# Kernel optimization log

Hardware: AMD Instinct MI355X
Metric: run time of the kernel (lower is better)

The kernel has to match this reference:

```python
import jax, jax.numpy as jnp
import numpy as np
import math

B, T, D_MODEL, H = 2, 2048, 1024, 16
HD = D_MODEL // H  # head_dim = 64


def setup_inputs() -> dict:
    key = jax.random.key(0)
    ks = jax.random.split(key, 9)
    inp = {
        "x_q": jax.random.normal(ks[0], (B, T, D_MODEL), dtype=jnp.float32),
        "x_k": jax.random.normal(ks[1], (B, T, D_MODEL), dtype=jnp.float32),
        "x_v": jax.random.normal(ks[2], (B, T, D_MODEL), dtype=jnp.float32),
        "mask": jax.random.randint(ks[3], (B, T), 0, 2, dtype=jnp.int32),
        "causal": 1,
        "relative_position_bias": jax.random.normal(ks[4], (1, H, T, T), dtype=jnp.float32),
        "Wq": jax.random.normal(ks[5], (D_MODEL, D_MODEL), dtype=jnp.float32) * 0.02,
        "Wk": jax.random.normal(ks[6], (D_MODEL, D_MODEL), dtype=jnp.float32) * 0.02,
        "Wv": jax.random.normal(ks[7], (D_MODEL, D_MODEL), dtype=jnp.float32) * 0.02,
        "Wo": jax.random.normal(ks[8], (D_MODEL, D_MODEL), dtype=jnp.float32) * 0.02,
    }
    return inp


def _split_heads(x):
    b, t, _ = x.shape
    return x.reshape(b, t, H, HD).transpose(0, 2, 1, 3)  # (B, H, T, HD)


def reference(x_q, x_k, x_v, mask, causal, relative_position_bias, Wq, Wk, Wv, Wo):
    # torch.nn.Linear: y = x @ W.T
    q = _split_heads(x_q @ Wq.T)
    k = _split_heads(x_k @ Wk.T)
    v = _split_heads(x_v @ Wv.T)

    # padding mask (B, T_k) -> (B, 1, 1, T_k), combined with causal tril
    attn_mask = mask[:, None, None, :]
    if causal:
        tril = jnp.tril(jnp.ones((T, T), dtype=jnp.int32))[None, None]
        attn_mask = attn_mask & tril

    scores = jnp.einsum('bhqd,bhkd->bhqk', q, k) / math.sqrt(HD)
    scores = scores + relative_position_bias
    scores = jnp.where(attn_mask == 0, jnp.float32(-1e9), scores)
    attn = jax.nn.softmax(scores, axis=-1)  # (B, H, Tq, Tk)

    out_h = jnp.einsum('bhqk,bhkd->bhqd', attn, v)
    out = out_h.transpose(0, 2, 1, 3).reshape(B, T, D_MODEL)
    out = out @ Wo.T
    return out, attn
```

## Files before the change

kernel.cpp:

```cpp
#include <hip/hip_runtime.h>
#include <hip/hip_bf16.h>
#include <hip/hip_fp16.h>

#define B_ 2
#define T_ 2048
#define DM 1024
#define H_ 16
#define HD_ 64

typedef __attribute__((ext_vector_type(8))) short bf16x8v;
typedef __attribute__((ext_vector_type(4))) short short4v;
typedef __attribute__((ext_vector_type(4))) float f32x4;

__device__ __forceinline__ short f2bf(float f){
  unsigned u = __builtin_bit_cast(unsigned, f);
  u += 0x7fffu + ((u >> 16) & 1u);
  return (short)(u >> 16);
}
__device__ __forceinline__ float bf2f(short s){
  unsigned u = ((unsigned)(unsigned short)s) << 16;
  return __builtin_bit_cast(float, u);
}

#define GLOAD_LDS16(g, l) \
  __builtin_amdgcn_global_load_lds((const __attribute__((address_space(1))) unsigned int*)(g), \
                                   (__attribute__((address_space(3))) unsigned int*)(l), 16, 0, 0)

#define MFMA16(a, b, c) __builtin_amdgcn_mfma_f32_16x16x32_bf16((a), (b), (c), 0, 0, 0)

__global__ __launch_bounds__(256) void conv_kernel(
    const float* __restrict__ s0, const float* __restrict__ s1, const float* __restrict__ s2,
    const float* __restrict__ s3, const float* __restrict__ s4, const float* __restrict__ s5,
    const float* __restrict__ s6,
    short* __restrict__ d0, short* __restrict__ d1, short* __restrict__ d2,
    short* __restrict__ d3, short* __restrict__ d4, short* __restrict__ d5,
    short* __restrict__ d6)
{
  int y = blockIdx.y;
  const float* s; short* d; int n;
  switch (y) {
    case 0: s = s0; d = d0; n = B_*T_*DM; break;
    case 1: s = s1; d = d1; n = B_*T_*DM; break;
    case 2: s = s2; d = d2; n = B_*T_*DM; break;
    case 3: s = s3; d = d3; n = DM*DM;   break;
    case 4: s = s4; d = d4; n = DM*DM;   break;
    case 5: s = s5; d = d5; n = DM*DM;   break;
    default: s = s6; d = d6; n = DM*DM;  break;
  }
  int i = (blockIdx.x * 256 + threadIdx.x) * 4;
  if (i >= n) return;
  float4 f = *(const float4*)(s + i);
  short4v o;
  o.x = f2bf(f.x); o.y = f2bf(f.y); o.z = f2bf(f.z); o.w = f2bf(f.w);
  *(short4v*)(d + i) = o;
}

__global__ __launch_bounds__(256) void proj_gemm(
    const short* __restrict__ xq, const short* __restrict__ xk, const short* __restrict__ xv,
    const short* __restrict__ wq, const short* __restrict__ wk, const short* __restrict__ wv,
    short* __restrict__ qo, short* __restrict__ ko, short* __restrict__ vto)
{
  __shared__ short As[128 * 32];
  __shared__ short Bs[128 * 32];
  const int z = blockIdx.z;
  const short* A  = (z == 0) ? xq : (z == 1) ? xk : xv;
  const short* Bw = (z == 0) ? wq : (z == 1) ? wk : wv;
  const int m0 = blockIdx.x * 128;
  const int n0 = blockIdx.y * 128;
  const int tid = threadIdx.x;
  const int w = tid >> 6, l = tid & 63;
  const int wr = w >> 1, wc = w & 1;
  const int fr = l & 15, kq8 = (l >> 4) * 8;
  const int srow = tid >> 2, scol = (tid & 3) * 8;

  f32x4 acc[4][4] = {};

  for (int k0 = 0; k0 < DM; k0 += 32) {
    __syncthreads();
    GLOAD_LDS16(A  + (size_t)(m0 + srow) * DM + k0 + scol,      (char*)As + tid * 16);
    GLOAD_LDS16(A  + (size_t)(m0 + 64 + srow) * DM + k0 + scol, (char*)As + 4096 + tid * 16);
    GLOAD_LDS16(Bw + (size_t)(n0 + srow) * DM + k0 + scol,      (char*)Bs + tid * 16);
    GLOAD_LDS16(Bw + (size_t)(n0 + 64 + srow) * DM + k0 + scol, (char*)Bs + 4096 + tid * 16);
    __syncthreads();
    bf16x8v a[4], b[4];
#pragma unroll
    for (int i = 0; i < 4; i++) a[i] = *(const bf16x8v*)&As[(wr * 64 + i * 16 + fr) * 32 + kq8];
#pragma unroll
    for (int j = 0; j < 4; j++) b[j] = *(const bf16x8v*)&Bs[(wc * 64 + j * 16 + fr) * 32 + kq8];
#pragma unroll
    for (int i = 0; i < 4; i++)
#pragma unroll
      for (int j = 0; j < 4; j++)
        acc[i][j] = MFMA16(a[i], b[j], acc[i][j]);
  }

  const float scale = (z == 0) ? 0.125f : 1.0f;
  short* dst01 = (z == 0) ? qo : ko;
#pragma unroll
  for (int i = 0; i < 4; i++) {
#pragma unroll
    for (int j = 0; j < 4; j++) {
#pragma unroll
      for (int r = 0; r < 4; r++) {
        int row = m0 + wr * 64 + i * 16 + (l >> 4) * 4 + r;
        int col = n0 + wc * 64 + j * 16 + fr;
        int bb = row >> 11, tt = row & (T_ - 1);
        int hh = col >> 6,  hd = col & (HD_ - 1);
        short v = f2bf(acc[i][j][r] * scale);
        if (z == 2)
          vto[(((size_t)bb * H_ + hh) * HD_ + hd) * T_ + tt] = v;
        else
          dst01[(((size_t)bb * H_ + hh) * T_ + tt) * HD_ + hd] = v;
      }
    }
  }
}

__global__ __launch_bounds__(256) void vsum_kernel(const short* __restrict__ vt,
                                                   float* __restrict__ vs)
{
  __shared__ float red[256];
  int bh = blockIdx.x;
  int tid = threadIdx.x;
  int hd = tid & 63, part = tid >> 6;
  const short* src = vt + ((size_t)bh * HD_ + hd) * T_ + part * 512;
  float s = 0.f;
  for (int i = 0; i < 512; i += 4) {
    short4v v = *(const short4v*)(src + i);
    s += bf2f(v.x) + bf2f(v.y) + bf2f(v.z) + bf2f(v.w);
  }
  red[tid] = s;
  __syncthreads();
  if (part == 0)
    vs[(size_t)bh * HD_ + hd] = red[hd] + red[64 + hd] + red[128 + hd] + red[192 + hd];
}

__global__ __launch_bounds__(128, 4) void attn_kernel(
    const short* __restrict__ qw, const short* __restrict__ kw, const short* __restrict__ vt,
    const float* __restrict__ bias, const int* __restrict__ mask,
    const int* __restrict__ causal_p, const float* __restrict__ vsum,
    float* __restrict__ attn_out, short* __restrict__ outh)
{
  __shared__ short p_l[2][2][16][68];
  __shared__ float ml_l[2][2][16][2];
  __shared__ float mrow_l[2][16];
  float* pv = (float*)&p_l[0][0][0][0];

  const int tid = threadIdx.x;
  const int w = tid >> 6, l = tid & 63;
  const int fr = l & 15, q4 = l >> 4, kq8 = q4 * 8;
  const int wgid = blockIdx.x;
  const int h  = (wgid & 7) | (((wgid >> 3) & 1) << 3);
  const int jt = 127 - (wgid >> 4);
  const int q0w = jt * 16;
  const int causal = *causal_p;
  const int L = causal ? (q0w + 16) : T_;
  const int KEND = (L + 63) & ~63;
  const float invT = 1.0f / (float)T_;
  const int qrow = q0w + fr;

  const short* Kb0 = kw + ((size_t)0 * H_ + h) * T_ * HD_;
  const short* Kb1 = kw + ((size_t)1 * H_ + h) * T_ * HD_;
  const short* Vb0 = vt + ((size_t)0 * H_ + h) * HD_ * T_;
  const short* Vb1 = vt + ((size_t)1 * H_ + h) * HD_ * T_;
  const float* brow = bias + ((size_t)h * T_ + qrow) * T_;

  bf16x8v qa[2][2];
#pragma unroll
  for (int b = 0; b < 2; b++) {
    const short* qp = qw + (((size_t)b * H_ + h) * T_ + qrow) * HD_;
    qa[b][0] = *(const bf16x8v*)(qp + kq8);
    qa[b][1] = *(const bf16x8v*)(qp + 32 + kq8);
  }

  float m_[2] = {-3e38f, -3e38f}, l_[2] = {0.f, 0.f};

  for (int k0 = w * 64; k0 < KEND; k0 += 128) {
    f32x4 sv[2][4];
#pragma unroll
    for (int t = 0; t < 4; t++) {
      const int kb = k0 + t * 16;
      const short* kp0 = Kb0 + (size_t)(kb + fr) * HD_ + kq8;
      const short* kp1 = Kb1 + (size_t)(kb + fr) * HD_ + kq8;
      f32x4 a0 = {0.f, 0.f, 0.f, 0.f}, a1 = {0.f, 0.f, 0.f, 0.f};
      a0 = MFMA16(*(const bf16x8v*)kp0,        qa[0][0], a0);
      a0 = MFMA16(*(const bf16x8v*)(kp0 + 32), qa[0][1], a0);
      a1 = MFMA16(*(const bf16x8v*)kp1,        qa[1][0], a1);
      a1 = MFMA16(*(const bf16x8v*)(kp1 + 32), qa[1][1], a1);
      f32x4 bi = *(const f32x4*)(brow + kb + q4 * 4);
      int4 mk0 = *(const int4*)(mask + kb + q4 * 4);
      int4 mk1 = *(const int4*)(mask + T_ + kb + q4 * 4);
      int mka[4] = {mk0.x, mk0.y, mk0.z, mk0.w};
      int mkb[4] = {mk1.x, mk1.y, mk1.z, mk1.w};
      if (!causal || (kb + 15 <= q0w)) {
#pragma unroll
        for (int r = 0; r < 4; r++) {
          sv[0][t][r] = mka[r] ? (a0[r] + bi[r]) : -1e9f;
          sv[1][t][r] = mkb[r] ? (a1[r] + bi[r]) : -1e9f;
        }
      } else {
#pragma unroll
        for (int r = 0; r < 4; r++) {
          bool cok = (kb + q4 * 4 + r) <= qrow;
          sv[0][t][r] = (mka[r] && cok) ? (a0[r] + bi[r]) : -1e9f;
          sv[1][t][r] = (mkb[r] && cok) ? (a1[r] + bi[r]) : -1e9f;
        }
      }
    }
#pragma unroll
    for (int b = 0; b < 2; b++) {
      float tm = -3e38f;
#pragma unroll
      for (int t = 0; t < 4; t++)
#pragma unroll
        for (int r = 0; r < 4; r++) tm = fmaxf(tm, sv[b][t][r]);
      float nm = fmaxf(m_[b], tm);
      float ss = 0.f;
#pragma unroll
      for (int t = 0; t < 4; t++)
#pragma unroll
        for (int r = 0; r < 4; r++) ss += __expf(sv[b][t][r] - nm);
      l_[b] = l_[b] * __expf(m_[b] - nm) + ss;
      m_[b] = nm;
    }
  }
#pragma unroll
  for (int b = 0; b < 2; b++) {
#pragma unroll
    for (int off = 16; off < 64; off <<= 1) {
      float om = __shfl_xor(m_[b], off);
      float ol = __shfl_xor(l_[b], off);
      float nm = fmaxf(m_[b], om);
      l_[b] = l_[b] * __expf(m_[b] - nm) + ol * __expf(om - nm);
      m_[b] = nm;
    }
  }
  if (q4 == 0) {
#pragma unroll
    for (int b = 0; b < 2; b++) {
      ml_l[w][b][fr][0] = m_[b];
      ml_l[w][b][fr][1] = l_[b];
    }
  }
  __syncthreads();

  float lse[2];
  bool fm[2];
#pragma unroll
  for (int b = 0; b < 2; b++) {
    float ma = ml_l[0][b][fr][0], la = ml_l[0][b][fr][1];
    float mb = ml_l[1][b][fr][0], lb = ml_l[1][b][fr][1];
    float M = fmaxf(ma, mb);
    float lsum = la * __expf(ma - M) + lb * __expf(mb - M);
    fm[b] = (M <= -0.5e9f);
    lse[b] = M + __logf(lsum);
    if (q4 == 0 && w == 0) mrow_l[b][fr] = M;
  }

  f32x4 oacc[2][4] = {};
  for (int k0 = w * 64; k0 < KEND; k0 += 128) {
#pragma unroll
    for (int t = 0; t < 4; t++) {
      const int kb = k0 + t * 16;
      const short* kp0 = Kb0 + (size_t)(kb + fr) * HD_ + kq8;
      const short* kp1 = Kb1 + (size_t)(kb + fr) * HD_ + kq8;
      f32x4 a0 = {0.f, 0.f, 0.f, 0.f}, a1 = {0.f, 0.f, 0.f, 0.f};
      a0 = MFMA16(*(const bf16x8v*)kp0,        qa[0][0], a0);
      a0 = MFMA16(*(const bf16x8v*)(kp0 + 32), qa[0][1], a0);
      a1 = MFMA16(*(const bf16x8v*)kp1,        qa[1][0], a1);
      a1 = MFMA16(*(const bf16x8v*)(kp1 + 32), qa[1][1], a1);
      f32x4 bi = *(const f32x4*)(brow + kb + q4 * 4);
      int4 mk0 = *(const int4*)(mask + kb + q4 * 4);
      int4 mk1 = *(const int4*)(mask + T_ + kb + q4 * 4);
      int mka[4] = {mk0.x, mk0.y, mk0.z, mk0.w};
      int mkb[4] = {mk1.x, mk1.y, mk1.z, mk1.w};
      f32x4 p0, p1;
      if (!causal || (kb + 15 <= q0w)) {
#pragma unroll
        for (int r = 0; r < 4; r++) {
          p0[r] = mka[r] ? __expf(a0[r] + bi[r] - lse[0]) : 0.f;
          p1[r] = mkb[r] ? __expf(a1[r] + bi[r] - lse[1]) : 0.f;
        }
      } else {
#pragma unroll
        for (int r = 0; r < 4; r++) {
          bool cok = (kb + q4 * 4 + r) <= qrow;
          p0[r] = (mka[r] && cok) ? __expf(a0[r] + bi[r] - lse[0]) : 0.f;
          p1[r] = (mkb[r] && cok) ? __expf(a1[r] + bi[r] - lse[1]) : 0.f;
        }
      }
      f32x4 st0, st1;
#pragma unroll
      for (int r = 0; r < 4; r++) {
        st0[r] = fm[0] ? invT : p0[r];
        st1[r] = fm[1] ? invT : p1[r];
      }
      __builtin_nontemporal_store(st0,
          (f32x4*)(attn_out + (((size_t)0 * H_ + h) * T_ + qrow) * T_ + kb + q4 * 4));
      __builtin_nontemporal_store(st1,
          (f32x4*)(attn_out + (((size_t)1 * H_ + h) * T_ + qrow) * T_ + kb + q4 * 4));
      short4v pb0, pb1;
#pragma unroll
      for (int r = 0; r < 4; r++) { pb0[r] = f2bf(p0[r]); pb1[r] = f2bf(p1[r]); }
      *(short4v*)&p_l[w][0][fr][t * 16 + q4 * 4] = pb0;
      *(short4v*)&p_l[w][1][fr][t * 16 + q4 * 4] = pb1;
    }
#pragma unroll
    for (int ks = 0; ks < 2; ks++) {
      bf16x8v pa0 = *(const bf16x8v*)&p_l[w][0][fr][ks * 32 + kq8];
      bf16x8v pa1 = *(const bf16x8v*)&p_l[w][1][fr][ks * 32 + kq8];
#pragma unroll
      for (int n0 = 0; n0 < 4; n0++) {
        bf16x8v vv0 = *(const bf16x8v*)&Vb0[(size_t)(n0 * 16 + fr) * T_ + k0 + ks * 32 + kq8];
        bf16x8v vv1 = *(const bf16x8v*)&Vb1[(size_t)(n0 * 16 + fr) * T_ + k0 + ks * 32 + kq8];
        oacc[0][n0] = MFMA16(pa0, vv0, oacc[0][n0]);
        oacc[1][n0] = MFMA16(pa1, vv1, oacc[1][n0]);
      }
    }
  }

  __syncthreads();
  if (w == 0) {
#pragma unroll
    for (int b = 0; b < 2; b++)
#pragma unroll
      for (int n0 = 0; n0 < 4; n0++)
#pragma unroll
        for (int r = 0; r < 4; r++)
          pv[(b * 16 + q4 * 4 + r) * 64 + n0 * 16 + fr] = oacc[b][n0][r];
  }
  __syncthreads();
  if (w == 1) {
#pragma unroll
    for (int b = 0; b < 2; b++)
#pragma unroll
      for (int n0 = 0; n0 < 4; n0++)
#pragma unroll
        for (int r = 0; r < 4; r++) {
          int row = q4 * 4 + r, col = n0 * 16 + fr;
          float val = oacc[b][n0][r] + pv[(b * 16 + row) * 64 + col];
          if (mrow_l[b][row] <= -0.5e9f)
            val = vsum[((size_t)b * H_ + h) * HD_ + col] * invT;
          outh[(((size_t)b * H_ + h) * T_ + q0w + row) * HD_ + col] = f2bf(val);
        }
  }

  if (KEND < T_) {
    float fill0 = fm[0] ? invT : 0.f;
    float fill1 = fm[1] ? invT : 0.f;
    f32x4 fv0 = {fill0, fill0, fill0, fill0};
    f32x4 fv1 = {fill1, fill1, fill1, fill1};
    float* r0 = attn_out + (((size_t)0 * H_ + h) * T_ + qrow) * T_;
    float* r1 = attn_out + (((size_t)1 * H_ + h) * T_ + qrow) * T_;
    for (int cb = KEND + w * 64; cb < T_; cb += 128) {
#pragma unroll
      for (int t = 0; t < 4; t++) {
        __builtin_nontemporal_store(fv0, (f32x4*)(r0 + cb + t * 16 + q4 * 4));
        __builtin_nontemporal_store(fv1, (f32x4*)(r1 + cb + t * 16 + q4 * 4));
      }
    }
  }
}

__global__ __launch_bounds__(256) void out_gemm(
    const short* __restrict__ Ah, const short* __restrict__ Bw, float* __restrict__ Co)
{
  __shared__ short As[128 * 32];
  __shared__ short Bs[128 * 32];
  const int m0 = blockIdx.x * 128;
  const int n0 = blockIdx.y * 128;
  const int tid = threadIdx.x;
  const int w = tid >> 6, l = tid & 63;
  const int wr = w >> 1, wc = w & 1;
  const int fr = l & 15, kq8 = (l >> 4) * 8;
  const int srow = tid >> 2, scol = (tid & 3) * 8;

  f32x4 acc[4][4] = {};

  for (int k0 = 0; k0 < DM; k0 += 32) {
    __syncthreads();
    int kk = k0 + scol;
    int hh = kk >> 6, hd = kk & 63;
    {
      int m1 = m0 + srow;
      const short* src1 = Ah + (((size_t)(m1 >> 11) * H_ + hh) * T_ + (m1 & (T_ - 1))) * HD_ + hd;
      GLOAD_LDS16(src1, (char*)As + tid * 16);
      int m2 = m0 + 64 + srow;
      const short* src2 = Ah + (((size_t)(m2 >> 11) * H_ + hh) * T_ + (m2 & (T_ - 1))) * HD_ + hd;
      GLOAD_LDS16(src2, (char*)As + 4096 + tid * 16);
    }
    GLOAD_LDS16(Bw + (size_t)(n0 + srow) * DM + kk,      (char*)Bs + tid * 16);
    GLOAD_LDS16(Bw + (size_t)(n0 + 64 + srow) * DM + kk, (char*)Bs + 4096 + tid * 16);
    __syncthreads();
    bf16x8v a[4], b[4];
#pragma unroll
    for (int i = 0; i < 4; i++) a[i] = *(const bf16x8v*)&As[(wr * 64 + i * 16 + fr) * 32 + kq8];
#pragma unroll
    for (int j = 0; j < 4; j++) b[j] = *(const bf16x8v*)&Bs[(wc * 64 + j * 16 + fr) * 32 + kq8];
#pragma unroll
    for (int i = 0; i < 4; i++)
#pragma unroll
      for (int j = 0; j < 4; j++)
        acc[i][j] = MFMA16(a[i], b[j], acc[i][j]);
  }

#pragma unroll
  for (int i = 0; i < 4; i++)
#pragma unroll
    for (int j = 0; j < 4; j++)
#pragma unroll
      for (int r = 0; r < 4; r++) {
        int row = m0 + wr * 64 + i * 16 + (l >> 4) * 4 + r;
        int col = n0 + wc * 64 + j * 16 + fr;
        Co[(size_t)row * DM + col] = acc[i][j][r];
      }
}

extern "C" void kernel_launch(void* const* d_in, const int* in_sizes, int n_in,
                              void* d_out, int out_size, void* d_ws, size_t ws_size,
                              hipStream_t stream)
{
  const float* x_q  = (const float*)d_in[0];
  const float* x_k  = (const float*)d_in[1];
  const float* x_v  = (const float*)d_in[2];
  const int*   mask = (const int*)d_in[3];
  const int*   causal = (const int*)d_in[4];
  const float* bias = (const float*)d_in[5];
  const float* Wq   = (const float*)d_in[6];
  const float* Wk   = (const float*)d_in[7];
  const float* Wv   = (const float*)d_in[8];
  const float* Wo   = (const float*)d_in[9];

  char* ws = (char*)d_ws;
  const size_t XB = (size_t)B_ * T_ * DM * 2;
  const size_t WB = (size_t)DM * DM * 2;
  short* xq_b = (short*)(ws + 0 * XB);
  short* xk_b = (short*)(ws + 1 * XB);
  short* xv_b = (short*)(ws + 2 * XB);
  short* wq_b = (short*)(ws + 3 * XB + 0 * WB);
  short* wk_b = (short*)(ws + 3 * XB + 1 * WB);
  short* wv_b = (short*)(ws + 3 * XB + 2 * WB);
  short* wo_b = (short*)(ws + 3 * XB + 3 * WB);
  short* q_ws  = (short*)(ws + 3 * XB + 4 * WB);
  short* k_ws  = (short*)(ws + 4 * XB + 4 * WB);
  short* vt_ws = (short*)(ws + 5 * XB + 4 * WB);
  short* oh_ws = (short*)(ws + 6 * XB + 4 * WB);
  float* vs_ws = (float*)(ws + 7 * XB + 4 * WB);

  float* out0 = (float*)d_out;
  float* attn = out0 + (size_t)B_ * T_ * DM;

  conv_kernel<<<dim3(4096, 7, 1), 256, 0, stream>>>(
      x_q, x_k, x_v, Wq, Wk, Wv, Wo,
      xq_b, xk_b, xv_b, wq_b, wk_b, wv_b, wo_b);

  proj_gemm<<<dim3(32, 8, 3), 256, 0, stream>>>(
      xq_b, xk_b, xv_b, wq_b, wk_b, wv_b, q_ws, k_ws, vt_ws);

  vsum_kernel<<<dim3(32, 1, 1), 256, 0, stream>>>(vt_ws, vs_ws);

  attn_kernel<<<dim3(2048, 1, 1), 128, 0, stream>>>(
      q_ws, k_ws, vt_ws, bias, mask, causal, vs_ws, attn, oh_ws);

  out_gemm<<<dim3(32, 8, 1), 256, 0, stream>>>(oh_ws, wo_b, out0);
}
```

Before: 455.8 us.

## Split attention key range across four waves per block instead of two

```diff
diff --git a/kernel.cpp b/kernel.cpp
--- a/kernel.cpp
+++ b/kernel.cpp
@@ -135,16 +135,16 @@
     vs[(size_t)bh * HD_ + hd] = red[hd] + red[64 + hd] + red[128 + hd] + red[192 + hd];
 }
 
-__global__ __launch_bounds__(128, 4) void attn_kernel(
+__global__ __launch_bounds__(256, 6) void attn_kernel(
     const short* __restrict__ qw, const short* __restrict__ kw, const short* __restrict__ vt,
     const float* __restrict__ bias, const int* __restrict__ mask,
     const int* __restrict__ causal_p, const float* __restrict__ vsum,
     float* __restrict__ attn_out, short* __restrict__ outh)
 {
-  __shared__ short p_l[2][2][16][68];
-  __shared__ float ml_l[2][2][16][2];
+  __shared__ short p_l[4][2][16][68];
+  __shared__ float ml_l[4][2][16][2];
   __shared__ float mrow_l[2][16];
-  float* pv = (float*)&p_l[0][0][0][0];
+  float* pvbuf = (float*)&p_l[0][0][0][0];
 
   const int tid = threadIdx.x;
   const int w = tid >> 6, l = tid & 63;
@@ -175,7 +175,7 @@
 
   float m_[2] = {-3e38f, -3e38f}, l_[2] = {0.f, 0.f};
 
-  for (int k0 = w * 64; k0 < KEND; k0 += 128) {
+  for (int k0 = w * 64; k0 < KEND; k0 += 256) {
     f32x4 sv[2][4];
 #pragma unroll
     for (int t = 0; t < 4; t++) {
@@ -248,17 +248,20 @@
   bool fm[2];
 #pragma unroll
   for (int b = 0; b < 2; b++) {
-    float ma = ml_l[0][b][fr][0], la = ml_l[0][b][fr][1];
-    float mb = ml_l[1][b][fr][0], lb = ml_l[1][b][fr][1];
-    float M = fmaxf(ma, mb);
-    float lsum = la * __expf(ma - M) + lb * __expf(mb - M);
+    float M = ml_l[0][b][fr][0];
+#pragma unroll
+    for (int w2 = 1; w2 < 4; w2++) M = fmaxf(M, ml_l[w2][b][fr][0]);
+    float lsum = 0.f;
+#pragma unroll
+    for (int w2 = 0; w2 < 4; w2++)
+      lsum += ml_l[w2][b][fr][1] * __expf(ml_l[w2][b][fr][0] - M);
     fm[b] = (M <= -0.5e9f);
     lse[b] = M + __logf(lsum);
     if (q4 == 0 && w == 0) mrow_l[b][fr] = M;
   }
 
   f32x4 oacc[2][4] = {};
-  for (int k0 = w * 64; k0 < KEND; k0 += 128) {
+  for (int k0 = w * 64; k0 < KEND; k0 += 256) {
 #pragma unroll
     for (int t = 0; t < 4; t++) {
       const int kb = k0 + t * 16;
@@ -320,29 +323,44 @@
   }
 
   __syncthreads();
-  if (w == 0) {
+  if (w >= 2) {
+    float* dst = pvbuf + (w - 2) * 2048;
 #pragma unroll
     for (int b = 0; b < 2; b++)
 #pragma unroll
       for (int n0 = 0; n0 < 4; n0++)
 #pragma unroll
         for (int r = 0; r < 4; r++)
-          pv[(b * 16 + q4 * 4 + r) * 64 + n0 * 16 + fr] = oacc[b][n0][r];
+          dst[(b * 16 + q4 * 4 + r) * 64 + n0 * 16 + fr] = oacc[b][n0][r];
   }
   __syncthreads();
-  if (w == 1) {
+  if (w < 2) {
+    float* dst = pvbuf + w * 2048;
 #pragma unroll
     for (int b = 0; b < 2; b++)
 #pragma unroll
       for (int n0 = 0; n0 < 4; n0++)
 #pragma unroll
         for (int r = 0; r < 4; r++) {
-          int row = q4 * 4 + r, col = n0 * 16 + fr;
-          float val = oacc[b][n0][r] + pv[(b * 16 + row) * 64 + col];
-          if (mrow_l[b][row] <= -0.5e9f)
-            val = vsum[((size_t)b * H_ + h) * HD_ + col] * invT;
-          outh[(((size_t)b * H_ + h) * T_ + q0w + row) * HD_ + col] = f2bf(val);
+          int idx = (b * 16 + q4 * 4 + r) * 64 + n0 * 16 + fr;
+          dst[idx] += oacc[b][n0][r];
         }
+  }
+  __syncthreads();
+  {
+    int b = tid >> 7, row = (tid >> 3) & 15, c0 = (tid & 7) * 8;
+    bool fmr = mrow_l[b][row] <= -0.5e9f;
+    int base = (b * 16 + row) * 64 + c0;
+    short4v o0, o1;
+#pragma unroll
+    for (int j = 0; j < 8; j++) {
+      float val = pvbuf[base + j] + pvbuf[2048 + base + j];
+      if (fmr) val = vsum[((size_t)b * H_ + h) * HD_ + c0 + j] * invT;
+      if (j < 4) o0[j] = f2bf(val); else o1[j - 4] = f2bf(val);
+    }
+    short* op = outh + (((size_t)b * H_ + h) * T_ + q0w + row) * HD_ + c0;
+    *(short4v*)op = o0;
+    *(short4v*)(op + 4) = o1;
   }
 
   if (KEND < T_) {
@@ -352,7 +370,7 @@
     f32x4 fv1 = {fill1, fill1, fill1, fill1};
     float* r0 = attn_out + (((size_t)0 * H_ + h) * T_ + qrow) * T_;
     float* r1 = attn_out + (((size_t)1 * H_ + h) * T_ + qrow) * T_;
-    for (int cb = KEND + w * 64; cb < T_; cb += 128) {
+    for (int cb = KEND + w * 64; cb < T_; cb += 256) {
 #pragma unroll
       for (int t = 0; t < 4; t++) {
         __builtin_nontemporal_store(fv0, (f32x4*)(r0 + cb + t * 16 + q4 * 4));
@@ -459,7 +477,7 @@
 
   vsum_kernel<<<dim3(32, 1, 1), 256, 0, stream>>>(vt_ws, vs_ws);
 
-  attn_kernel<<<dim3(2048, 1, 1), 128, 0, stream>>>(
+  attn_kernel<<<dim3(2048, 1, 1), 256, 0, stream>>>(
       q_ws, k_ws, vt_ws, bias, mask, causal, vs_ws, attn, oh_ws);
 
   out_gemm<<<dim3(32, 8, 1), 256, 0, stream>>>(oh_ws, wo_b, out0);
```

Result: slower. 687.2 us (+50.8%).

## Pair early and late query rows per workgroup to balance causal attention work

Applied to the files above, without the earlier changes.

```diff
diff --git a/kernel.cpp b/kernel.cpp
--- a/kernel.cpp
+++ b/kernel.cpp
@@ -151,13 +151,14 @@
   const int fr = l & 15, q4 = l >> 4, kq8 = q4 * 8;
   const int wgid = blockIdx.x;
   const int h  = (wgid & 7) | (((wgid >> 3) & 1) << 3);
-  const int jt = 127 - (wgid >> 4);
-  const int q0w = jt * 16;
+  const int jA = wgid >> 4;
+  const int q0A = jA * 8;
+  const int q0B = (255 - jA) * 8;
   const int causal = *causal_p;
-  const int L = causal ? (q0w + 16) : T_;
-  const int KEND = (L + 63) & ~63;
+  const int LB = q0B + 8;
+  const int KEND = causal ? ((LB + 63) & ~63) : T_;
   const float invT = 1.0f / (float)T_;
-  const int qrow = q0w + fr;
+  const int qrow = (fr < 8) ? (q0A + fr) : (q0B + fr - 8);
 
   const short* Kb0 = kw + ((size_t)0 * H_ + h) * T_ * HD_;
   const short* Kb1 = kw + ((size_t)1 * H_ + h) * T_ * HD_;
@@ -187,24 +188,18 @@
       a0 = MFMA16(*(const bf16x8v*)(kp0 + 32), qa[0][1], a0);
       a1 = MFMA16(*(const bf16x8v*)kp1,        qa[1][0], a1);
       a1 = MFMA16(*(const bf16x8v*)(kp1 + 32), qa[1][1], a1);
-      f32x4 bi = *(const f32x4*)(brow + kb + q4 * 4);
+      f32x4 bi = {0.f, 0.f, 0.f, 0.f};
+      if (!causal || (kb + q4 * 4 <= qrow))
+        bi = *(const f32x4*)(brow + kb + q4 * 4);
       int4 mk0 = *(const int4*)(mask + kb + q4 * 4);
       int4 mk1 = *(const int4*)(mask + T_ + kb + q4 * 4);
       int mka[4] = {mk0.x, mk0.y, mk0.z, mk0.w};
       int mkb[4] = {mk1.x, mk1.y, mk1.z, mk1.w};
-      if (!causal || (kb + 15 <= q0w)) {
-#pragma unroll
-        for (int r = 0; r < 4; r++) {
-          sv[0][t][r] = mka[r] ? (a0[r] + bi[r]) : -1e9f;
-          sv[1][t][r] = mkb[r] ? (a1[r] + bi[r]) : -1e9f;
-        }
-      } else {
-#pragma unroll
-        for (int r = 0; r < 4; r++) {
-          bool cok = (kb + q4 * 4 + r) <= qrow;
-          sv[0][t][r] = (mka[r] && cok) ? (a0[r] + bi[r]) : -1e9f;
-          sv[1][t][r] = (mkb[r] && cok) ? (a1[r] + bi[r]) : -1e9f;
-        }
+#pragma unroll
+      for (int r = 0; r < 4; r++) {
+        bool cok = (!causal) || ((kb + q4 * 4 + r) <= qrow);
+        sv[0][t][r] = (mka[r] && cok) ? (a0[r] + bi[r]) : -1e9f;
+        sv[1][t][r] = (mkb[r] && cok) ? (a1[r] + bi[r]) : -1e9f;
       }
     }
 #pragma unroll
@@ -269,25 +264,19 @@
       a0 = MFMA16(*(const bf16x8v*)(kp0 + 32), qa[0][1], a0);
       a1 = MFMA16(*(const bf16x8v*)kp1,        qa[1][0], a1);
       a1 = MFMA16(*(const bf16x8v*)(kp1 + 32), qa[1][1], a1);
-      f32x4 bi = *(const f32x4*)(brow + kb + q4 * 4);
+      f32x4 bi = {0.f, 0.f, 0.f, 0.f};
+      if (!causal || (kb + q4 * 4 <= qrow))
+        bi = *(const f32x4*)(brow + kb + q4 * 4);
       int4 mk0 = *(const int4*)(mask + kb + q4 * 4);
       int4 mk1 = *(const int4*)(mask + T_ + kb + q4 * 4);
       int mka[4] = {mk0.x, mk0.y, mk0.z, mk0.w};
       int mkb[4] = {mk1.x, mk1.y, mk1.z, mk1.w};
       f32x4 p0, p1;
-      if (!causal || (kb + 15 <= q0w)) {
-#pragma unroll
-        for (int r = 0; r < 4; r++) {
-          p0[r] = mka[r] ? __expf(a0[r] + bi[r] - lse[0]) : 0.f;
-          p1[r] = mkb[r] ? __expf(a1[r] + bi[r] - lse[1]) : 0.f;
-        }
-      } else {
-#pragma unroll
-        for (int r = 0; r < 4; r++) {
-          bool cok = (kb + q4 * 4 + r) <= qrow;
-          p0[r] = (mka[r] && cok) ? __expf(a0[r] + bi[r] - lse[0]) : 0.f;
-          p1[r] = (mkb[r] && cok) ? __expf(a1[r] + bi[r] - lse[1]) : 0.f;
-        }
+#pragma unroll
+      for (int r = 0; r < 4; r++) {
+        bool cok = (!causal) || ((kb + q4 * 4 + r) <= qrow);
+        p0[r] = (mka[r] && cok) ? __expf(a0[r] + bi[r] - lse[0]) : 0.f;
+        p1[r] = (mkb[r] && cok) ? __expf(a1[r] + bi[r] - lse[1]) : 0.f;
       }
       f32x4 st0, st1;
 #pragma unroll
@@ -338,10 +327,11 @@
 #pragma unroll
         for (int r = 0; r < 4; r++) {
           int row = q4 * 4 + r, col = n0 * 16 + fr;
+          int qg = (row < 8) ? (q0A + row) : (q0B + row - 8);
           float val = oacc[b][n0][r] + pv[(b * 16 + row) * 64 + col];
           if (mrow_l[b][row] <= -0.5e9f)
             val = vsum[((size_t)b * H_ + h) * HD_ + col] * invT;
-          outh[(((size_t)b * H_ + h) * T_ + q0w + row) * HD_ + col] = f2bf(val);
+          outh[(((size_t)b * H_ + h) * T_ + qg) * HD_ + col] = f2bf(val);
         }
   }
 
```

After: 467.5 us. 2.6% more time.
